# Optimization experiments

Hardware: AMD Instinct MI355X
Metric: run time of the kernel (lower is better)

The kernel has to match this reference:

```python
import jax, jax.numpy as jnp
import numpy as np

EMBED_DIM = 1024
NUM_HEADS = 16
HEAD_DIM = EMBED_DIM // NUM_HEADS


def setup_inputs() -> dict:
    key = jax.random.key(0)
    ks = jax.random.split(key, 6)
    s = 1.0 / np.sqrt(EMBED_DIM)
    return {
        "x": jax.random.normal(ks[0], (4, 2048, EMBED_DIM), dtype=jnp.float32),
        "Wq": jax.random.uniform(ks[1], (EMBED_DIM, EMBED_DIM), jnp.float32, -s, s),
        "Wk": jax.random.uniform(ks[2], (EMBED_DIM, EMBED_DIM), jnp.float32, -s, s),
        "Wv": jax.random.uniform(ks[3], (EMBED_DIM, EMBED_DIM), jnp.float32, -s, s),
        "Wo": jax.random.uniform(ks[4], (EMBED_DIM, EMBED_DIM), jnp.float32, -s, s),
        "bo": jax.random.uniform(ks[5], (EMBED_DIM,), jnp.float32, -s, s),
    }


def reference(x, Wq, Wk, Wv, Wo, bo):
    B, S, E = x.shape
    H, D = NUM_HEADS, HEAD_DIM
    # torch Linear: x @ W.T ; reshape to [B, H, S, D]
    q = (x @ Wq.T).reshape(B, S, H, D).transpose(0, 2, 1, 3)
    k = (x @ Wk.T).reshape(B, S, H, D).transpose(0, 2, 1, 3)
    v = (x @ Wv.T).reshape(B, S, H, D).transpose(0, 2, 1, 3)
    scores = jnp.einsum("bhqd,bhkd->bhqk", q, k) / jnp.sqrt(jnp.float32(D))
    attn = jax.nn.softmax(scores, axis=-1)  # dropout is identity in eval mode
    out = jnp.einsum("bhqk,bhkd->bhqd", attn, v)
    out = out.transpose(0, 2, 1, 3).reshape(B, S, E)
    return out @ Wo.T + bo
```

## Files before the change

kernel.cpp:

```cpp
#include <hip/hip_runtime.h>
#include <hip/hip_bf16.h>
#include <math.h>

#define B_ 4
#define S_ 2048
#define E_ 1024
#define H_ 16
#define D_ 64
#define M_ (B_*S_)
#define NKV 32

typedef __attribute__((ext_vector_type(8))) short short8;
typedef __attribute__((ext_vector_type(4))) short short4_t;
typedef __attribute__((ext_vector_type(4))) float f32x4;
typedef __attribute__((ext_vector_type(16))) float f32x16;

static __device__ __forceinline__ short f2bf(float f){
  union { float f; unsigned u; } v; v.f = f;
  unsigned u = v.u + 0x7FFFu + ((v.u >> 16) & 1u);
  return (short)(u >> 16);
}

__global__ void cast_all(const float* __restrict__ x,
    const float* __restrict__ wq, const float* __restrict__ wk,
    const float* __restrict__ wv, const float* __restrict__ wo,
    short8* __restrict__ xb, short8* __restrict__ wqb, short8* __restrict__ wkb,
    short8* __restrict__ wvb, short8* __restrict__ wob){
  int bid = blockIdx.x;
  const float* src; short8* dst; int i;
  if (bid < 4096) { src = x; dst = xb; i = bid*256 + threadIdx.x; }
  else {
    int k = (bid - 4096) >> 9;
    i = ((bid - 4096) & 511)*256 + threadIdx.x;
    src = k==0 ? wq : k==1 ? wk : k==2 ? wv : wo;
    dst = k==0 ? wqb : k==1 ? wkb : k==2 ? wvb : wob;
  }
  const float4* s4 = (const float4*)src;
  float4 a = s4[2*i], b = s4[2*i+1];
  short8 o;
  o[0]=f2bf(a.x); o[1]=f2bf(a.y); o[2]=f2bf(a.z); o[3]=f2bf(a.w);
  o[4]=f2bf(b.x); o[5]=f2bf(b.y); o[6]=f2bf(b.z); o[7]=f2bf(b.w);
  dst[i]=o;
}

#define GLOAD16(g, l) __builtin_amdgcn_global_load_lds( \
    (const __attribute__((address_space(1))) void*)(g), \
    (__attribute__((address_space(3))) void*)(l), 16, 0, 0)

__global__ __launch_bounds__(512,2) void gemm_qkv(const short* __restrict__ A,
      const short* __restrict__ Wf, short* __restrict__ Qo, short* __restrict__ Ko,
      short* __restrict__ Vto, float u)
{
  extern __shared__ char LDSc[];
  const int tid = threadIdx.x;
  const int w = tid >> 6, lane = tid & 63;
  const int l15 = lane & 15, l4 = lane >> 4;
  const int rx = l15 & 7;
  const int wm = w >> 2, wn = w & 3;
  const int m0 = blockIdx.x * 256;
  const int n0 = blockIdx.y * 256;

  const int lanerow = lane >> 3;
  const int lchunk8 = ((lane & 7) ^ lanerow) * 8;
  const short* Aq = A  + (size_t)(m0 + w*8 + lanerow)*1024 + lchunk8;
  const short* Bq = Wf + (size_t)(n0 + w*8 + lanerow)*1024 + lchunk8;

  #define STA(kt,h,i) GLOAD16(Aq + (size_t)((h)*128 + (i)*64)*1024 + (kt)*64, \
      LDSc + ((kt)&1)*65536 + (h)*16384 + (i)*8192 + w*1024);
  #define STB(kt,h,i) GLOAD16(Bq + (size_t)((h)*128 + (i)*64)*1024 + (kt)*64, \
      LDSc + ((kt)&1)*65536 + 32768 + (h)*16384 + (i)*8192 + w*1024);

  #define BARF __builtin_amdgcn_s_barrier(); \
               asm volatile("" ::: "memory"); \
               __builtin_amdgcn_sched_barrier(0);

  f32x4 acc[8][4] = {};

  STA(0,0,0) STA(0,0,1) STA(0,1,0) STA(0,1,1)
  STB(0,0,0) STB(0,0,1) STB(0,1,0) STB(0,1,1)
  asm volatile("s_waitcnt vmcnt(0)" ::: "memory");
  BARF

  #define RDA(QM) \
    _Pragma("unroll") for (int i_ = 0; i_ < 4; ++i_) \
    _Pragma("unroll") for (int ks_ = 0; ks_ < 2; ++ks_) \
      af_[i_][ks_] = *(const short8*)(Ab + (wm*128 + (QM)*64 + i_*16 + l15)*128 + (((ks_*4 + l4) ^ rx)*16));
  #define RDB(DST,QN) \
    _Pragma("unroll") for (int j_ = 0; j_ < 2; ++j_) \
    _Pragma("unroll") for (int ks_ = 0; ks_ < 2; ++ks_) \
      DST[j_][ks_] = *(const short8*)(Bb + (wn*64 + (QN)*32 + j_*16 + l15)*128 + (((ks_*4 + l4) ^ rx)*16));
  #define MF(QM,QN,BF) \
    __builtin_amdgcn_s_setprio(1); \
    _Pragma("unroll") for (int i_ = 0; i_ < 4; ++i_) \
    _Pragma("unroll") for (int j_ = 0; j_ < 2; ++j_) \
    _Pragma("unroll") for (int ks_ = 0; ks_ < 2; ++ks_) \
      acc[(QM)*4+i_][(QN)*2+j_] = __builtin_amdgcn_mfma_f32_16x16x32_bf16( \
          af_[i_][ks_], BF[j_][ks_], acc[(QM)*4+i_][(QN)*2+j_], 0,0,0); \
    __builtin_amdgcn_s_setprio(0);

  for (int k = 0; k < 16; ++k) {
    const char* Ab = LDSc + (k & 1)*65536;
    const char* Bb = Ab + 32768;
    const bool st = (k < 15);
    short8 af_[4][2], b0_[2][2], b1_[2][2];
    RDA(0)
    RDB(b0_, 0)
    if (st) { STA(k+1,0,0) STA(k+1,0,1) STA(k+1,1,0) STA(k+1,1,1) }
    BARF
    MF(0,0,b0_)
    BARF
    RDB(b1_, 1)
    if (st) { STB(k+1,0,0) STB(k+1,0,1) }
    BARF
    MF(0,1,b1_)
    BARF
    RDA(1)
    if (st) { STB(k+1,1,0) STB(k+1,1,1) }
    BARF
    MF(1,1,b1_)
    BARF
    MF(1,0,b0_)
    asm volatile("s_waitcnt vmcnt(0)" ::: "memory");
    BARF
  }
  #undef RDA
  #undef RDB
  #undef MF
  #undef STA
  #undef STB

  const int sel = n0 >> 10;
  const int ncb = (n0 & 1023) + wn*64;
  if (sel == 2) {
    #pragma unroll
    for (int i = 0; i < 8; ++i) {
      int row = m0 + wm*128 + i*16 + 4*l4;
      int b = row >> 11;
      int s0 = row & 2047;
      #pragma unroll
      for (int j = 0; j < 4; ++j) {
        int col = ncb + j*16 + l15;
        int h = col >> 6, d = col & 63;
        short4_t pk;
        pk[0]=f2bf(acc[i][j][0]); pk[1]=f2bf(acc[i][j][1]);
        pk[2]=f2bf(acc[i][j][2]); pk[3]=f2bf(acc[i][j][3]);
        *(short4_t*)(Vto + (((size_t)(b*H_ + h))*D_ + d)*S_ + s0) = pk;
      }
    }
  } else {
    short* O = sel ? Ko : Qo;
    float sc = sel ? 1.0f : u;
    #pragma unroll
    for (int i = 0; i < 8; ++i) {
      int row = m0 + wm*128 + i*16 + 4*l4;
      int b = row >> 11;
      #pragma unroll
      for (int j = 0; j < 4; ++j) {
        int col = ncb + j*16 + l15;
        int h = col >> 6, d = col & 63;
        #pragma unroll
        for (int r = 0; r < 4; ++r) {
          int s = (row + r) & 2047;
          O[(((size_t)(b*H_ + h))*S_ + s)*D_ + d] = f2bf(acc[i][j][r]*sc);
        }
      }
    }
  }
  #undef BARF
}

__global__ __launch_bounds__(256,2) void gemm_out(const short* __restrict__ A,
      const short* __restrict__ W, float* __restrict__ out,
      const float* __restrict__ bias)
{
  __shared__ short AL[128*32];
  __shared__ short BL[128*32];
  const int tid = threadIdx.x;
  const int w = tid >> 6, lane = tid & 63;
  const int l15 = lane & 15, l4 = lane >> 4;
  const int m0 = blockIdx.x * 128;
  const int n0 = blockIdx.y * 128;
  const int wr = w >> 1, wc = w & 1;
  f32x4 acc[4][4] = {};

  const short* ga = A + (size_t)(m0 + (tid>>2))*1024 + (tid&3)*8;
  const short* gb = W + (size_t)(n0 + (tid>>2))*1024 + (tid&3)*8;

  for (int kt = 0; kt < 32; ++kt) {
    const int ko = kt*32;
    #pragma unroll
    for (int p = 0; p < 2; ++p) {
      GLOAD16(ga + (size_t)(p*64)*1024 + ko, (char*)AL + p*4096 + w*1024);
      GLOAD16(gb + (size_t)(p*64)*1024 + ko, (char*)BL + p*4096 + w*1024);
    }
    __syncthreads();
    short8 af[4], bw[4];
    #pragma unroll
    for (int i = 0; i < 4; ++i) {
      af[i] = *(const short8*)(AL + (wr*64 + i*16 + l15)*32 + 8*l4);
      bw[i] = *(const short8*)(BL + (wc*64 + i*16 + l15)*32 + 8*l4);
    }
    #pragma unroll
    for (int i = 0; i < 4; ++i)
      #pragma unroll
      for (int j = 0; j < 4; ++j)
        acc[i][j] = __builtin_amdgcn_mfma_f32_16x16x32_bf16(af[i], bw[j], acc[i][j], 0,0,0);
    __syncthreads();
  }

  #pragma unroll
  for (int i = 0; i < 4; ++i) {
    int row = m0 + wr*64 + i*16 + 4*l4;
    #pragma unroll
    for (int j = 0; j < 4; ++j) {
      int col = n0 + wc*64 + j*16 + l15;
      float bz = bias[col];
      #pragma unroll
      for (int r = 0; r < 4; ++r)
        out[(size_t)(row + r)*1024 + col] = acc[i][j][r] + bz;
    }
  }
}

static __device__ __forceinline__ unsigned cvtpk(float lo, float hi){
  unsigned d; asm("v_cvt_pk_bf16_f32 %0, %1, %2" : "=v"(d) : "v"(lo), "v"(hi)); return d;
}
static __device__ __forceinline__ void plswap(unsigned &a, unsigned &b){
  asm("v_permlane32_swap_b32 %0, %1" : "+v"(a), "+v"(b));
}
template<int BASE>
static __device__ __forceinline__ short8 pfrag(const f32x16 &s){
  unsigned w01 = cvtpk(s[BASE+0], s[BASE+1]);
  unsigned w23 = cvtpk(s[BASE+2], s[BASE+3]);
  unsigned w45 = cvtpk(s[BASE+4], s[BASE+5]);
  unsigned w67 = cvtpk(s[BASE+6], s[BASE+7]);
  plswap(w01, w45);
  plswap(w23, w67);
  union { unsigned u[4]; short8 s8; } r;
  r.u[0]=w01; r.u[1]=w23; r.u[2]=w45; r.u[3]=w67;
  return r.s8;
}

__global__ __launch_bounds__(256,4) void attn_kernel(const short* __restrict__ Qb,
    const short* __restrict__ Kb, const short* __restrict__ Vtb, short* __restrict__ Ob)
{
  __shared__ short KL[2][64*64];
  __shared__ short VL[2][64*64];
  const int tid = threadIdx.x, w = tid >> 6, lane = tid & 63;
  const int l31 = lane & 31, hi = lane >> 5;
  const int rx7 = l31 & 7;

  const int linear = blockIdx.x;
  const int swz = (linear & 7)*128 + (linear >> 3);
  const int bh = swz >> 4;
  const int b = bh >> 4, h = bh & 15;
  const int q0 = (swz & 15) * 128;

  const short* Qg = Qb + ((size_t)bh*S_ + q0)*D_;
  const short* Kg = Kb + (size_t)bh*S_*D_;
  const short* Vg = Vtb + (size_t)bh*D_*S_;

  const int srow = tid >> 3;
  const int scol = ((tid & 7) ^ (srow & 7)) * 8;

  #define STAGE(t, bi) { \
    GLOAD16(Kg + (size_t)((t)*64 +      srow)*D_ + scol, (char*)KL[bi] + w*1024); \
    GLOAD16(Kg + (size_t)((t)*64 + 32 + srow)*D_ + scol, (char*)KL[bi] + 4096 + w*1024); \
    GLOAD16(Vg + (size_t)(     srow)*S_ + (t)*64 + scol, (char*)VL[bi] + w*1024); \
    GLOAD16(Vg + (size_t)(32 + srow)*S_ + (t)*64 + scol, (char*)VL[bi] + 4096 + w*1024); }

  STAGE(0, 0)

  const int qrow = w*32 + l31;
  short8 qf[4];
  #pragma unroll
  for (int t = 0; t < 4; ++t)
    qf[t] = *(const short8*)(Qg + (size_t)qrow*D_ + (2*t + hi)*8);

  f32x16 oacc[2] = {};
  float l_run = 0.f;

  for (int kv = 0; kv < NKV; ++kv) {
    const int cur = kv & 1;
    if (kv < NKV-1) {
      STAGE(kv+1, cur^1)
      asm volatile("s_waitcnt vmcnt(4)" ::: "memory");
    } else {
      asm volatile("s_waitcnt vmcnt(0)" ::: "memory");
    }
    __builtin_amdgcn_s_barrier();
    asm volatile("" ::: "memory");
    __builtin_amdgcn_sched_barrier(0);

    f32x16 st[2] = {};
    __builtin_amdgcn_s_setprio(1);
    #pragma unroll
    for (int t = 0; t < 4; ++t) {
      int co = ((2*t + hi) ^ rx7)*16;
      short8 ka0 = *(const short8*)((char*)KL[cur] + l31*128 + co);
      short8 ka1 = *(const short8*)((char*)KL[cur] + (32 + l31)*128 + co);
      st[0] = __builtin_amdgcn_mfma_f32_32x32x16_bf16(ka0, qf[t], st[0], 0,0,0);
      st[1] = __builtin_amdgcn_mfma_f32_32x32x16_bf16(ka1, qf[t], st[1], 0,0,0);
    }
    __builtin_amdgcn_s_setprio(0);

    #pragma unroll
    for (int r = 0; r < 16; ++r) st[0][r] = __builtin_amdgcn_exp2f(st[0][r]);
    #pragma unroll
    for (int r = 0; r < 16; ++r) st[1][r] = __builtin_amdgcn_exp2f(st[1][r]);
    {
      f32x16 sv = st[0] + st[1];
      float sa = (sv[0]+sv[1]) + (sv[2]+sv[3]);
      float sb = (sv[4]+sv[5]) + (sv[6]+sv[7]);
      float sc = (sv[8]+sv[9]) + (sv[10]+sv[11]);
      float sd = (sv[12]+sv[13]) + (sv[14]+sv[15]);
      l_run += (sa+sb) + (sc+sd);
    }

    short8 pf[4];
    pf[0] = pfrag<0>(st[0]);
    pf[1] = pfrag<8>(st[0]);
    pf[2] = pfrag<0>(st[1]);
    pf[3] = pfrag<8>(st[1]);

    __builtin_amdgcn_s_setprio(1);
    #pragma unroll
    for (int t = 0; t < 4; ++t) {
      int co = ((2*t + hi) ^ rx7)*16;
      short8 va0 = *(const short8*)((char*)VL[cur] + l31*128 + co);
      short8 va1 = *(const short8*)((char*)VL[cur] + (32 + l31)*128 + co);
      oacc[0] = __builtin_amdgcn_mfma_f32_32x32x16_bf16(va0, pf[t], oacc[0], 0,0,0);
      oacc[1] = __builtin_amdgcn_mfma_f32_32x32x16_bf16(va1, pf[t], oacc[1], 0,0,0);
    }
    __builtin_amdgcn_s_setprio(0);
    __builtin_amdgcn_sched_barrier(0);
    asm volatile("" ::: "memory");
    __builtin_amdgcn_s_barrier();
    asm volatile("" ::: "memory");
  }
  #undef STAGE

  float lt = l_run + __shfl_xor(l_run, 32);
  float inv = 1.f / lt;
  int s = q0 + qrow;
  short* orow = Ob + ((size_t)(b*S_ + s))*E_ + h*64;
  #pragma unroll
  for (int r = 0; r < 16; r += 2) {
    int d0 = (r & 3) + 8*(r >> 2) + 4*hi;
    unsigned pa = (unsigned short)f2bf(oacc[0][r]*inv) |
                  ((unsigned)(unsigned short)f2bf(oacc[0][r+1]*inv) << 16);
    unsigned pb = (unsigned short)f2bf(oacc[1][r]*inv) |
                  ((unsigned)(unsigned short)f2bf(oacc[1][r+1]*inv) << 16);
    *(unsigned*)(orow + d0) = pa;
    *(unsigned*)(orow + 32 + d0) = pb;
  }
}

extern "C" void kernel_launch(void* const* d_in, const int* in_sizes, int n_in,
                              void* d_out, int out_size, void* d_ws, size_t ws_size,
                              hipStream_t stream) {
  const float* x  = (const float*)d_in[0];
  const float* Wq = (const float*)d_in[1];
  const float* Wk = (const float*)d_in[2];
  const float* Wv = (const float*)d_in[3];
  const float* Wo = (const float*)d_in[4];
  const float* bo = (const float*)d_in[5];

  char* ws = (char*)d_ws;
  short* xb  = (short*)(ws);
  short* Wqb = (short*)(ws + (16u<<20));
  short* Wkb = (short*)(ws + (18u<<20));
  short* Wvb = (short*)(ws + (20u<<20));
  short* Wob = (short*)(ws + (22u<<20));
  short* Qb  = (short*)(ws + (24u<<20));
  short* Kb  = (short*)(ws + (40u<<20));
  short* Vtb = (short*)(ws + (56u<<20));
  short* Ab  = (short*)(ws + (72u<<20));

  cast_all<<<4096 + 4*512, 256, 0, stream>>>(x, Wq, Wk, Wv, Wo,
      (short8*)xb, (short8*)Wqb, (short8*)Wkb, (short8*)Wvb, (short8*)Wob);

  const float u = 0.18033688011112042f;
  gemm_qkv<<<dim3(32, 12), 512, 131072, stream>>>(xb, Wqb, Qb, Kb, Vtb, u);

  attn_kernel<<<1024, 256, 0, stream>>>(Qb, Kb, Vtb, Ab);

  gemm_out<<<dim3(64, 8), 256, 0, stream>>>(Ab, Wob, (float*)d_out, bo);
}
```

Measured before the change: 185.6 us.

## Process two query tiles per wave in attention to reuse K/V LDS loads

```diff
diff --git a/kernel.cpp b/kernel.cpp
--- a/kernel.cpp
+++ b/kernel.cpp
@@ -241,7 +241,7 @@
   return r.s8;
 }
 
-__global__ __launch_bounds__(256,4) void attn_kernel(const short* __restrict__ Qb,
+__global__ __launch_bounds__(256,2) void attn_kernel(const short* __restrict__ Qb,
     const short* __restrict__ Kb, const short* __restrict__ Vtb, short* __restrict__ Ob)
 {
   __shared__ short KL[2][64*64];
@@ -251,10 +251,10 @@
   const int rx7 = l31 & 7;
 
   const int linear = blockIdx.x;
-  const int swz = (linear & 7)*128 + (linear >> 3);
-  const int bh = swz >> 4;
+  const int swz = (linear & 7)*64 + (linear >> 3);
+  const int bh = swz >> 3;
   const int b = bh >> 4, h = bh & 15;
-  const int q0 = (swz & 15) * 128;
+  const int q0 = (swz & 7) * 256;
 
   const short* Qg = Qb + ((size_t)bh*S_ + q0)*D_;
   const short* Kg = Kb + (size_t)bh*S_*D_;
@@ -271,14 +271,15 @@
 
   STAGE(0, 0)
 
-  const int qrow = w*32 + l31;
-  short8 qf[4];
+  short8 qf[2][4];
   #pragma unroll
-  for (int t = 0; t < 4; ++t)
-    qf[t] = *(const short8*)(Qg + (size_t)qrow*D_ + (2*t + hi)*8);
-
-  f32x16 oacc[2] = {};
-  float l_run = 0.f;
+  for (int qt = 0; qt < 2; ++qt)
+    #pragma unroll
+    for (int t = 0; t < 4; ++t)
+      qf[qt][t] = *(const short8*)(Qg + (size_t)(w*64 + qt*32 + l31)*D_ + (2*t + hi)*8);
+
+  f32x16 oacc[2][2] = {};
+  float l_run[2] = {0.f, 0.f};
 
   for (int kv = 0; kv < NKV; ++kv) {
     const int cur = kv & 1;
@@ -292,36 +293,41 @@
     asm volatile("" ::: "memory");
     __builtin_amdgcn_sched_barrier(0);
 
-    f32x16 st[2] = {};
+    f32x16 st[2][2] = {};
     __builtin_amdgcn_s_setprio(1);
     #pragma unroll
     for (int t = 0; t < 4; ++t) {
       int co = ((2*t + hi) ^ rx7)*16;
       short8 ka0 = *(const short8*)((char*)KL[cur] + l31*128 + co);
       short8 ka1 = *(const short8*)((char*)KL[cur] + (32 + l31)*128 + co);
-      st[0] = __builtin_amdgcn_mfma_f32_32x32x16_bf16(ka0, qf[t], st[0], 0,0,0);
-      st[1] = __builtin_amdgcn_mfma_f32_32x32x16_bf16(ka1, qf[t], st[1], 0,0,0);
+      #pragma unroll
+      for (int qt = 0; qt < 2; ++qt) {
+        st[qt][0] = __builtin_amdgcn_mfma_f32_32x32x16_bf16(ka0, qf[qt][t], st[qt][0], 0,0,0);
+        st[qt][1] = __builtin_amdgcn_mfma_f32_32x32x16_bf16(ka1, qf[qt][t], st[qt][1], 0,0,0);
+      }
     }
     __builtin_amdgcn_s_setprio(0);
 
-    #pragma unroll
-    for (int r = 0; r < 16; ++r) st[0][r] = __builtin_amdgcn_exp2f(st[0][r]);
-    #pragma unroll
-    for (int r = 0; r < 16; ++r) st[1][r] = __builtin_amdgcn_exp2f(st[1][r]);
-    {
-      f32x16 sv = st[0] + st[1];
-      float sa = (sv[0]+sv[1]) + (sv[2]+sv[3]);
-      float sb = (sv[4]+sv[5]) + (sv[6]+sv[7]);
-      float sc = (sv[8]+sv[9]) + (sv[10]+sv[11]);
-      float sd = (sv[12]+sv[13]) + (sv[14]+sv[15]);
-      l_run += (sa+sb) + (sc+sd);
-    }
-
-    short8 pf[4];
-    pf[0] = pfrag<0>(st[0]);
-    pf[1] = pfrag<8>(st[0]);
-    pf[2] = pfrag<0>(st[1]);
-    pf[3] = pfrag<8>(st[1]);
+    short8 pf[2][4];
+    #pragma unroll
+    for (int qt = 0; qt < 2; ++qt) {
+      #pragma unroll
+      for (int r = 0; r < 16; ++r) st[qt][0][r] = __builtin_amdgcn_exp2f(st[qt][0][r]);
+      #pragma unroll
+      for (int r = 0; r < 16; ++r) st[qt][1][r] = __builtin_amdgcn_exp2f(st[qt][1][r]);
+      {
+        f32x16 sv = st[qt][0] + st[qt][1];
+        float sa = (sv[0]+sv[1]) + (sv[2]+sv[3]);
+        float sb = (sv[4]+sv[5]) + (sv[6]+sv[7]);
+        float sc = (sv[8]+sv[9]) + (sv[10]+sv[11]);
+        float sd = (sv[12]+sv[13]) + (sv[14]+sv[15]);
+        l_run[qt] += (sa+sb) + (sc+sd);
+      }
+      pf[qt][0] = pfrag<0>(st[qt][0]);
+      pf[qt][1] = pfrag<8>(st[qt][0]);
+      pf[qt][2] = pfrag<0>(st[qt][1]);
+      pf[qt][3] = pfrag<8>(st[qt][1]);
+    }
 
     __builtin_amdgcn_s_setprio(1);
     #pragma unroll
@@ -329,8 +335,11 @@
       int co = ((2*t + hi) ^ rx7)*16;
       short8 va0 = *(const short8*)((char*)VL[cur] + l31*128 + co);
       short8 va1 = *(const short8*)((char*)VL[cur] + (32 + l31)*128 + co);
-      oacc[0] = __builtin_amdgcn_mfma_f32_32x32x16_bf16(va0, pf[t], oacc[0], 0,0,0);
-      oacc[1] = __builtin_amdgcn_mfma_f32_32x32x16_bf16(va1, pf[t], oacc[1], 0,0,0);
+      #pragma unroll
+      for (int qt = 0; qt < 2; ++qt) {
+        oacc[qt][0] = __builtin_amdgcn_mfma_f32_32x32x16_bf16(va0, pf[qt][t], oacc[qt][0], 0,0,0);
+        oacc[qt][1] = __builtin_amdgcn_mfma_f32_32x32x16_bf16(va1, pf[qt][t], oacc[qt][1], 0,0,0);
+      }
     }
     __builtin_amdgcn_s_setprio(0);
     __builtin_amdgcn_sched_barrier(0);
@@ -340,19 +349,22 @@
   }
   #undef STAGE
 
-  float lt = l_run + __shfl_xor(l_run, 32);
-  float inv = 1.f / lt;
-  int s = q0 + qrow;
-  short* orow = Ob + ((size_t)(b*S_ + s))*E_ + h*64;
   #pragma unroll
-  for (int r = 0; r < 16; r += 2) {
-    int d0 = (r & 3) + 8*(r >> 2) + 4*hi;
-    unsigned pa = (unsigned short)f2bf(oacc[0][r]*inv) |
-                  ((unsigned)(unsigned short)f2bf(oacc[0][r+1]*inv) << 16);
-    unsigned pb = (unsigned short)f2bf(oacc[1][r]*inv) |
-                  ((unsigned)(unsigned short)f2bf(oacc[1][r+1]*inv) << 16);
-    *(unsigned*)(orow + d0) = pa;
-    *(unsigned*)(orow + 32 + d0) = pb;
+  for (int qt = 0; qt < 2; ++qt) {
+    float lt = l_run[qt] + __shfl_xor(l_run[qt], 32);
+    float inv = 1.f / lt;
+    int s = q0 + w*64 + qt*32 + l31;
+    short* orow = Ob + ((size_t)(b*S_ + s))*E_ + h*64;
+    #pragma unroll
+    for (int r = 0; r < 16; r += 2) {
+      int d0 = (r & 3) + 8*(r >> 2) + 4*hi;
+      unsigned pa = (unsigned short)f2bf(oacc[qt][0][r]*inv) |
+                    ((unsigned)(unsigned short)f2bf(oacc[qt][0][r+1]*inv) << 16);
+      unsigned pb = (unsigned short)f2bf(oacc[qt][1][r]*inv) |
+                    ((unsigned)(unsigned short)f2bf(oacc[qt][1][r+1]*inv) << 16);
+      *(unsigned*)(orow + d0) = pa;
+      *(unsigned*)(orow + 32 + d0) = pb;
+    }
   }
 }
 
@@ -383,7 +395,7 @@
   const float u = 0.18033688011112042f;
   gemm_qkv<<<dim3(32, 12), 512, 131072, stream>>>(xb, Wqb, Qb, Kb, Vtb, u);
 
-  attn_kernel<<<1024, 256, 0, stream>>>(Qb, Kb, Vtb, Ab);
+  attn_kernel<<<512, 256, 0, stream>>>(Qb, Kb, Vtb, Ab);
 
   gemm_out<<<dim3(64, 8), 256, 0, stream>>>(Ab, Wob, (float*)d_out, bo);
 }
```

Measured after the change: 184.1 us. Within noise of the previous version (-0.8%).

## Retile QKV GEMM to 256x192 blocks for a 512-block grid

Applied to the files above, without the earlier changes.

```diff
diff --git a/kernel.cpp b/kernel.cpp
--- a/kernel.cpp
+++ b/kernel.cpp
@@ -47,7 +47,7 @@
     (const __attribute__((address_space(1))) void*)(g), \
     (__attribute__((address_space(3))) void*)(l), 16, 0, 0)
 
-__global__ __launch_bounds__(512,2) void gemm_qkv(const short* __restrict__ A,
+__global__ __launch_bounds__(512,1) void gemm_qkv(const short* __restrict__ A,
       const short* __restrict__ Wf, short* __restrict__ Qo, short* __restrict__ Ko,
       short* __restrict__ Vto, float u)
 {
@@ -58,26 +58,26 @@
   const int rx = l15 & 7;
   const int wm = w >> 2, wn = w & 3;
   const int m0 = blockIdx.x * 256;
-  const int n0 = blockIdx.y * 256;
+  const int n0 = blockIdx.y * 192;
 
   const int lanerow = lane >> 3;
   const int lchunk8 = ((lane & 7) ^ lanerow) * 8;
   const short* Aq = A  + (size_t)(m0 + w*8 + lanerow)*1024 + lchunk8;
   const short* Bq = Wf + (size_t)(n0 + w*8 + lanerow)*1024 + lchunk8;
 
-  #define STA(kt,h,i) GLOAD16(Aq + (size_t)((h)*128 + (i)*64)*1024 + (kt)*64, \
-      LDSc + ((kt)&1)*65536 + (h)*16384 + (i)*8192 + w*1024);
-  #define STB(kt,h,i) GLOAD16(Bq + (size_t)((h)*128 + (i)*64)*1024 + (kt)*64, \
-      LDSc + ((kt)&1)*65536 + 32768 + (h)*16384 + (i)*8192 + w*1024);
+  #define STA(kt,i) GLOAD16(Aq + (size_t)((i)*64)*1024 + (kt)*64, \
+      LDSc + ((kt)&1)*57344 + (i)*8192 + w*1024);
+  #define STB(kt,i) GLOAD16(Bq + (size_t)((i)*64)*1024 + (kt)*64, \
+      LDSc + ((kt)&1)*57344 + 32768 + (i)*8192 + w*1024);
 
   #define BARF __builtin_amdgcn_s_barrier(); \
                asm volatile("" ::: "memory"); \
                __builtin_amdgcn_sched_barrier(0);
 
-  f32x4 acc[8][4] = {};
-
-  STA(0,0,0) STA(0,0,1) STA(0,1,0) STA(0,1,1)
-  STB(0,0,0) STB(0,0,1) STB(0,1,0) STB(0,1,1)
+  f32x4 acc[8][3] = {};
+
+  STA(0,0) STA(0,1) STA(0,2) STA(0,3)
+  STB(0,0) STB(0,1) STB(0,2)
   asm volatile("s_waitcnt vmcnt(0)" ::: "memory");
   BARF
 
@@ -85,41 +85,34 @@
     _Pragma("unroll") for (int i_ = 0; i_ < 4; ++i_) \
     _Pragma("unroll") for (int ks_ = 0; ks_ < 2; ++ks_) \
       af_[i_][ks_] = *(const short8*)(Ab + (wm*128 + (QM)*64 + i_*16 + l15)*128 + (((ks_*4 + l4) ^ rx)*16));
-  #define RDB(DST,QN) \
-    _Pragma("unroll") for (int j_ = 0; j_ < 2; ++j_) \
+  #define RDB \
+    _Pragma("unroll") for (int j_ = 0; j_ < 3; ++j_) \
     _Pragma("unroll") for (int ks_ = 0; ks_ < 2; ++ks_) \
-      DST[j_][ks_] = *(const short8*)(Bb + (wn*64 + (QN)*32 + j_*16 + l15)*128 + (((ks_*4 + l4) ^ rx)*16));
-  #define MF(QM,QN,BF) \
+      bf_[j_][ks_] = *(const short8*)(Bb + (wn*48 + j_*16 + l15)*128 + (((ks_*4 + l4) ^ rx)*16));
+  #define MF(QM) \
     __builtin_amdgcn_s_setprio(1); \
     _Pragma("unroll") for (int i_ = 0; i_ < 4; ++i_) \
-    _Pragma("unroll") for (int j_ = 0; j_ < 2; ++j_) \
+    _Pragma("unroll") for (int j_ = 0; j_ < 3; ++j_) \
     _Pragma("unroll") for (int ks_ = 0; ks_ < 2; ++ks_) \
-      acc[(QM)*4+i_][(QN)*2+j_] = __builtin_amdgcn_mfma_f32_16x16x32_bf16( \
-          af_[i_][ks_], BF[j_][ks_], acc[(QM)*4+i_][(QN)*2+j_], 0,0,0); \
+      acc[(QM)*4+i_][j_] = __builtin_amdgcn_mfma_f32_16x16x32_bf16( \
+          af_[i_][ks_], bf_[j_][ks_], acc[(QM)*4+i_][j_], 0,0,0); \
     __builtin_amdgcn_s_setprio(0);
 
   for (int k = 0; k < 16; ++k) {
-    const char* Ab = LDSc + (k & 1)*65536;
+    const char* Ab = LDSc + (k & 1)*57344;
     const char* Bb = Ab + 32768;
     const bool st = (k < 15);
-    short8 af_[4][2], b0_[2][2], b1_[2][2];
+    short8 af_[4][2], bf_[3][2];
     RDA(0)
-    RDB(b0_, 0)
-    if (st) { STA(k+1,0,0) STA(k+1,0,1) STA(k+1,1,0) STA(k+1,1,1) }
+    RDB
+    if (st) { STA(k+1,0) STA(k+1,1) STA(k+1,2) STA(k+1,3) }
     BARF
-    MF(0,0,b0_)
-    BARF
-    RDB(b1_, 1)
-    if (st) { STB(k+1,0,0) STB(k+1,0,1) }
-    BARF
-    MF(0,1,b1_)
+    MF(0)
     BARF
     RDA(1)
-    if (st) { STB(k+1,1,0) STB(k+1,1,1) }
+    if (st) { STB(k+1,0) STB(k+1,1) STB(k+1,2) }
     BARF
-    MF(1,1,b1_)
-    BARF
-    MF(1,0,b0_)
+    MF(1)
     asm volatile("s_waitcnt vmcnt(0)" ::: "memory");
     BARF
   }
@@ -128,45 +121,35 @@
   #undef MF
   #undef STA
   #undef STB
-
-  const int sel = n0 >> 10;
-  const int ncb = (n0 & 1023) + wn*64;
-  if (sel == 2) {
-    #pragma unroll
-    for (int i = 0; i < 8; ++i) {
-      int row = m0 + wm*128 + i*16 + 4*l4;
-      int b = row >> 11;
-      int s0 = row & 2047;
-      #pragma unroll
-      for (int j = 0; j < 4; ++j) {
-        int col = ncb + j*16 + l15;
-        int h = col >> 6, d = col & 63;
+  #undef BARF
+
+  #pragma unroll
+  for (int i = 0; i < 8; ++i) {
+    int row = m0 + wm*128 + i*16 + 4*l4;
+    int b = row >> 11;
+    int s0 = row & 2047;
+    #pragma unroll
+    for (int j = 0; j < 3; ++j) {
+      int col = n0 + wn*48 + j*16 + l15;
+      int sel = col >> 10;
+      int colm = col & 1023;
+      int h = colm >> 6, d = colm & 63;
+      if (sel == 2) {
         short4_t pk;
         pk[0]=f2bf(acc[i][j][0]); pk[1]=f2bf(acc[i][j][1]);
         pk[2]=f2bf(acc[i][j][2]); pk[3]=f2bf(acc[i][j][3]);
         *(short4_t*)(Vto + (((size_t)(b*H_ + h))*D_ + d)*S_ + s0) = pk;
-      }
-    }
-  } else {
-    short* O = sel ? Ko : Qo;
-    float sc = sel ? 1.0f : u;
-    #pragma unroll
-    for (int i = 0; i < 8; ++i) {
-      int row = m0 + wm*128 + i*16 + 4*l4;
-      int b = row >> 11;
-      #pragma unroll
-      for (int j = 0; j < 4; ++j) {
-        int col = ncb + j*16 + l15;
-        int h = col >> 6, d = col & 63;
+      } else {
+        short* O = sel ? Ko : Qo;
+        float sc = sel ? 1.0f : u;
         #pragma unroll
         for (int r = 0; r < 4; ++r) {
-          int s = (row + r) & 2047;
+          int s = (s0 + r) & 2047;
           O[(((size_t)(b*H_ + h))*S_ + s)*D_ + d] = f2bf(acc[i][j][r]*sc);
         }
       }
     }
   }
-  #undef BARF
 }
 
 __global__ __launch_bounds__(256,2) void gemm_out(const short* __restrict__ A,
@@ -381,7 +364,7 @@
       (short8*)xb, (short8*)Wqb, (short8*)Wkb, (short8*)Wvb, (short8*)Wob);
 
   const float u = 0.18033688011112042f;
-  gemm_qkv<<<dim3(32, 12), 512, 131072, stream>>>(xb, Wqb, Qb, Kb, Vtb, u);
+  gemm_qkv<<<dim3(32, 16), 512, 114688, stream>>>(xb, Wqb, Qb, Kb, Vtb, u);
 
   attn_kernel<<<1024, 256, 0, stream>>>(Qb, Kb, Vtb, Ab);
 
```

After: 178.2 us. -4.0%, faster.
